# Optimization experiments

Hardware: AMD Instinct MI355X
Metric: run time of the kernel (lower is better)

Reference implementation:

```python
import jax, jax.numpy as jnp
import numpy as np

B, N, TOP_K = 4, 2048, 30
NUM_PE, NUM_RBF, EDGE_F = 16, 16, 128

def l2norm(x, eps=1e-12):
    return x / jnp.maximum(jnp.linalg.norm(x, axis=-1, keepdims=True), eps)

def gather_nodes(nodes, idx):
    # nodes [B,N,C], idx [B,N,K] -> [B,N,K,C]
    return jax.vmap(lambda n, i: n[i])(nodes, idx)

def setup_inputs() -> dict:
    key = jax.random.key(0)
    k1, k2 = jax.random.split(key)
    X = jax.random.normal(k1, (B, N, 3), dtype=jnp.float32) * 5.0
    mask = jnp.ones((B, N), dtype=jnp.float32)
    W = jax.random.normal(k2, (NUM_PE + NUM_RBF + 7, EDGE_F), dtype=jnp.float32) * 0.1
    b = jnp.zeros((EDGE_F,), dtype=jnp.float32)
    gamma = jnp.ones((EDGE_F,), dtype=jnp.float32)
    beta = jnp.zeros((EDGE_F,), dtype=jnp.float32)
    return {"X": X, "mask": mask, "W": W, "b": b, "gamma": gamma, "beta": beta}

def _quaternions(R):
    # R [B,N,K,3,3] -> Q [B,N,K,4]
    diag = jnp.diagonal(R, axis1=-2, axis2=-1)  # [B,N,K,3]
    Rxx, Ryy, Rzz = diag[..., 0], diag[..., 1], diag[..., 2]
    mags = 0.5 * jnp.sqrt(jnp.abs(1.0 + jnp.stack(
        [Rxx - Ryy - Rzz, -Rxx + Ryy - Rzz, -Rxx - Ryy + Rzz], -1)))
    signs = jnp.sign(jnp.stack([
        R[..., 2, 1] - R[..., 1, 2],
        R[..., 0, 2] - R[..., 2, 0],
        R[..., 1, 0] - R[..., 0, 1]], -1))
    xyz = signs * mags
    w = jnp.sqrt(jax.nn.relu(1.0 + jnp.sum(diag, -1, keepdims=True))) / 2.0
    Q = jnp.concatenate((xyz, w), -1)
    return l2norm(Q)

def _forward(X, mask, W, b, gamma, beta):
    eps = 1e-6
    # pairwise distances + top-k neighbors
    mask_2D = mask[:, None, :] * mask[:, :, None]
    dXp = X[:, None, :, :] - X[:, :, None, :]
    D = mask_2D * jnp.sqrt(jnp.sum(dXp ** 2, -1) + eps)
    D_max = jnp.max(D, -1, keepdims=True)
    D_adjust = D + (1.0 - mask_2D) * D_max
    neg_vals, E_idx = jax.lax.top_k(-D_adjust, TOP_K)
    D_neighbors = -neg_vals

    # RBF
    D_mu = jnp.linspace(0.0, 20.0, NUM_RBF)
    D_sigma = 20.0 / NUM_RBF
    RBF = jnp.exp(-(((D_neighbors[..., None] - D_mu) / D_sigma) ** 2))

    # orientations
    dX = X[:, 1:, :] - X[:, :-1, :]
    U = l2norm(dX)
    u_2, u_1 = U[:, :-2, :], U[:, 1:-1, :]
    n_2 = l2norm(jnp.cross(u_2, u_1))
    o_1 = l2norm(u_2 - u_1)
    O = jnp.stack((o_1, n_2, jnp.cross(o_1, n_2)), 2)  # [B,N-3,3,3]
    O9 = O.reshape(O.shape[0], O.shape[1], 9)
    O9 = jnp.pad(O9, ((0, 0), (1, 2), (0, 0)))  # [B,N,9]
    O_neighbors = gather_nodes(O9, E_idx).reshape(B, N, TOP_K, 3, 3)
    X_neighbors = gather_nodes(X, E_idx)  # [B,N,K,3]
    Om = O9.reshape(B, N, 3, 3)
    dXn = X_neighbors - X[:, :, None, :]
    dU = l2norm(jnp.einsum('bnij,bnkj->bnki', Om, dXn))
    R = jnp.einsum('bnji,bnkjl->bnkil', Om, O_neighbors)
    Q = _quaternions(R)
    O_features = jnp.concatenate((dU, Q), -1)  # [B,N,K,7]

    # positional encodings
    ii = jnp.arange(N, dtype=jnp.float32)[None, :, None]
    d = (E_idx.astype(jnp.float32) - ii)[..., None]
    freq = jnp.exp(jnp.arange(0, NUM_PE, 2, dtype=jnp.float32) * -(np.log(10000.0) / NUM_PE))
    angles = d * freq
    E_positional = jnp.concatenate((jnp.cos(angles), jnp.sin(angles)), -1)

    E = jnp.concatenate((E_positional, RBF, O_features), -1)  # [B,N,K,39]
    E = E @ W + b
    # Normalize (LayerNorm w/ unbiased std, as in struct2seq Normalize)
    mu = jnp.mean(E, -1, keepdims=True)
    sigma = jnp.sqrt(jnp.var(E, -1, keepdims=True, ddof=1) + eps)
    E = gamma * (E - mu) / (sigma + eps) + beta
    return E, E_idx

def reference(X, mask, W, b, gamma, beta):
    return _forward(X, mask, W, b, gamma, beta)
```

## Files before the change

kernel.cpp:

```cpp
#include <hip/hip_runtime.h>
#include <stdint.h>

#define B_ 4
#define N_ 2048
#define K_ 30
#define F_ 128
#define NF 39

typedef unsigned long long u64;
typedef float f32x4 __attribute__((ext_vector_type(4)));
typedef short s16x8 __attribute__((ext_vector_type(8)));

__device__ __forceinline__ u64 umin64(u64 a, u64 b) { return a < b ? a : b; }
__device__ __forceinline__ u64 umax64(u64 a, u64 b) { return a > b ? a : b; }

template <int CTRL>
__device__ __forceinline__ float dpp_add(float x) {
    int r = __builtin_amdgcn_update_dpp(0, __float_as_int(x), CTRL, 0xF, 0xF, true);
    return x + __int_as_float(r);
}
__device__ __forceinline__ float rowsum16(float x) {
    x = dpp_add<0xB1>(x);
    x = dpp_add<0x4E>(x);
    x = dpp_add<0x141>(x);
    x = dpp_add<0x140>(x);
    return x;
}

__device__ __forceinline__ unsigned int bf16rne(float f) {
    unsigned int u = __float_as_uint(f);
    return (u + 0x7FFFu + ((u >> 16) & 1u)) >> 16;
}
__device__ __forceinline__ unsigned int bfpack(float a, float b) {
    return bf16rne(a) | (bf16rne(b) << 16);
}

__global__ __launch_bounds__(256) void topk_kernel(const float* __restrict__ X,
                                                   float* __restrict__ O9,
                                                   int* __restrict__ Eidx,
                                                   float* __restrict__ Dn,
                                                   float* __restrict__ EidxF) {
    __shared__ float4 P[N_];
    __shared__ u64 surv[4][64];
    int t = threadIdx.x, lane = t & 63, wid = t >> 6;
    int node = blockIdx.x * 4 + wid;
    int i = node & (N_ - 1);
    const float* Xb = X + (size_t)(node - i) * 3;
    float* Pf = (float*)P;

    for (int idx = t; idx < 3 * N_; idx += 256) {
        float v = Xb[idx];
        int j = idx / 3, c = idx - 3 * j;
        Pf[4 * j + c] = v;
    }
    __syncthreads();

    if (t < 4) {
        int nn = blockIdx.x * 4 + t;
        int ii = nn & (N_ - 1);
        float o[9] = {0.f,0.f,0.f,0.f,0.f,0.f,0.f,0.f,0.f};
        if (ii >= 1 && ii <= N_ - 3) {
            float4 A = P[ii-1], Bv = P[ii], C = P[ii+1];
            float u2x = Bv.x-A.x, u2y = Bv.y-A.y, u2z = Bv.z-A.z;
            float n2_ = sqrtf(u2x*u2x+u2y*u2y+u2z*u2z);
            float inv = 1.0f / fmaxf(n2_, 1e-12f);
            u2x*=inv; u2y*=inv; u2z*=inv;
            float u1x = C.x-Bv.x, u1y = C.y-Bv.y, u1z = C.z-Bv.z;
            float n1_ = sqrtf(u1x*u1x+u1y*u1y+u1z*u1z);
            inv = 1.0f / fmaxf(n1_, 1e-12f);
            u1x*=inv; u1y*=inv; u1z*=inv;
            float nx = u2y*u1z - u2z*u1y;
            float ny = u2z*u1x - u2x*u1z;
            float nz = u2x*u1y - u2y*u1x;
            float nn2 = sqrtf(nx*nx+ny*ny+nz*nz);
            inv = 1.0f / fmaxf(nn2, 1e-12f);
            nx*=inv; ny*=inv; nz*=inv;
            float ox = u2x-u1x, oy = u2y-u1y, oz = u2z-u1z;
            float no = sqrtf(ox*ox+oy*oy+oz*oz);
            inv = 1.0f / fmaxf(no, 1e-12f);
            ox*=inv; oy*=inv; oz*=inv;
            o[0]=ox; o[1]=oy; o[2]=oz;
            o[3]=nx; o[4]=ny; o[5]=nz;
            o[6]=oy*nz - oz*ny; o[7]=oz*nx - ox*nz; o[8]=ox*ny - oy*nx;
        }
        float* dst = O9 + (size_t)nn * 9;
        #pragma unroll
        for (int q = 0; q < 9; ++q) dst[q] = o[q];
    }

    float4 ci = P[i];
    float xi = ci.x, yi = ci.y, zi = ci.z;

    unsigned int d[32];
    #pragma unroll
    for (int s = 0; s < 32; ++s) {
        float4 p = P[lane + (s << 6)];
        float dx = __fsub_rn(p.x, xi);
        float dy = __fsub_rn(p.y, yi);
        float dz = __fsub_rn(p.z, zi);
        float s1 = __fadd_rn(__fmul_rn(dx,dx), __fmul_rn(dy,dy));
        float s2 = __fadd_rn(s1, __fmul_rn(dz,dz));
        d[s] = __float_as_uint(__fadd_rn(s2, 1e-6f));
    }

    unsigned int lm = d[0];
    #pragma unroll
    for (int s = 1; s < 32; ++s) lm = min(lm, d[s]);

    unsigned int v32 = lm;
    #pragma unroll
    for (int k = 2; k <= 64; k <<= 1) {
        #pragma unroll
        for (int j = k >> 1; j >= 1; j >>= 1) {
            unsigned int o = (unsigned int)__shfl_xor((int)v32, j, 64);
            bool up = ((lane & k) == 0);
            bool lower = ((lane & j) == 0);
            v32 = (lower == up) ? min(v32, o) : max(v32, o);
        }
    }
    unsigned int Bcut = (unsigned int)__shfl((int)v32, K_ - 1, 64) + 64u;

    surv[wid][lane] = ~0ull;
    int base = 0;
    #pragma unroll
    for (int s = 0; s < 32; ++s) {
        bool p = (d[s] <= Bcut);
        u64 blt = __ballot(p);
        if (p) {
            int slot = base + (int)__popcll(blt & ((1ull << lane) - 1ull));
            if (slot < 64) {
                float D = __fsqrt_rn(__uint_as_float(d[s]));
                surv[wid][slot] = (((u64)__float_as_uint(D)) << 32)
                                | (unsigned int)(lane + (s << 6));
            }
        }
        base += (int)__popcll(blt);
    }
    int cnt = base;

    if (cnt <= 64) {
        u64 v = surv[wid][lane];
        #pragma unroll
        for (int k = 2; k <= 64; k <<= 1) {
            #pragma unroll
            for (int j = k >> 1; j >= 1; j >>= 1) {
                u64 o = (u64)__shfl_xor((long long)v, j, 64);
                bool up = ((lane & k) == 0);
                bool lower = ((lane & j) == 0);
                v = (lower == up) ? umin64(v, o) : umax64(v, o);
            }
        }
        if (lane < K_ && lane < cnt) {
            int j = (int)(v & 0xffffffffull);
            int o = node * K_ + lane;
            Eidx[o] = j;
            Dn[o] = __uint_as_float((unsigned int)(v >> 32));
            EidxF[o] = (float)j;
        }
    } else {
        #pragma unroll
        for (int s = 0; s < 32; ++s)
            d[s] = __float_as_uint(__fsqrt_rn(__uint_as_float(d[s])));
        for (int k = 0; k < K_; ++k) {
            u64 m = ~0ull;
            #pragma unroll
            for (int s = 0; s < 32; ++s) {
                u64 kk = (((u64)d[s]) << 32) | (unsigned int)(lane + (s << 6));
                m = umin64(m, kk);
            }
            #pragma unroll
            for (int off = 1; off < 64; off <<= 1)
                m = umin64(m, (u64)__shfl_xor((long long)m, off, 64));
            #pragma unroll
            for (int s = 0; s < 32; ++s) {
                u64 kk = (((u64)d[s]) << 32) | (unsigned int)(lane + (s << 6));
                if (kk == m) d[s] = 0xFFFFFFFFu;
            }
            if (lane == 0) {
                int o = node * K_ + k;
                int j = (int)(m & 0xffffffffull);
                Eidx[o] = j;
                Dn[o] = __uint_as_float((unsigned int)(m >> 32));
                EidxF[o] = (float)j;
            }
        }
    }
}

__global__ __launch_bounds__(256) void edge_fused(const float* __restrict__ X,
                                                  const float* __restrict__ O9,
                                                  const int* __restrict__ Eidx,
                                                  const float* __restrict__ Dn,
                                                  const float* __restrict__ W,
                                                  const float* __restrict__ bias,
                                                  const float* __restrict__ gamma,
                                                  const float* __restrict__ beta,
                                                  float* __restrict__ E) {
    __shared__ unsigned int ldsF[128 * 32];
    __shared__ unsigned int ldsW[128 * 32];
    int t = threadIdx.x, lane = t & 63, wid = t >> 6;
    int e0 = blockIdx.x * 128;

    if (t < 128) {
        int e = e0 + t;
        int b = e / (N_ * K_);
        int rem = e - b * (N_ * K_);
        int i = rem / K_;
        int node = b * N_ + i;
        int j = Eidx[e];
        float dnb = Dn[e];

        float f[40];
        float dd = (float)(j - i);
        const float freqs[8] = {1.0f, 0.31622776601683794f, 0.1f, 0.031622776601683794f,
                                0.01f, 0.0031622776601683794f, 0.001f, 0.00031622776601683794f};
        #pragma unroll
        for (int l = 0; l < 8; ++l) {
            float a = dd * freqs[l];
            float sv, cv;
            __sincosf(a, &sv, &cv);
            f[l] = cv;
            f[8 + l] = sv;
        }
        #pragma unroll
        for (int r = 0; r < 16; ++r) {
            float mu = (20.0f / 15.0f) * (float)r;
            float u = (dnb - mu) * 0.8f;
            f[16 + r] = __expf(-u * u);
        }
        const float* Omp = O9 + (size_t)node * 9;
        float Om[9];
        #pragma unroll
        for (int q = 0; q < 9; ++q) Om[q] = Omp[q];
        const float* Xi = X + (size_t)node * 3;
        const float* Xj = X + (size_t)(b * N_ + j) * 3;
        float dx = Xj[0] - Xi[0], dy = Xj[1] - Xi[1], dz = Xj[2] - Xi[2];
        float v0 = Om[0]*dx + Om[1]*dy + Om[2]*dz;
        float v1 = Om[3]*dx + Om[4]*dy + Om[5]*dz;
        float v2 = Om[6]*dx + Om[7]*dy + Om[8]*dz;
        float n = sqrtf(v0*v0 + v1*v1 + v2*v2);
        float inv = 1.0f / fmaxf(n, 1e-12f);
        f[32] = v0 * inv; f[33] = v1 * inv; f[34] = v2 * inv;
        const float* On = O9 + (size_t)(b * N_ + j) * 9;
        float R00 = Om[0]*On[0] + Om[3]*On[3] + Om[6]*On[6];
        float R01 = Om[0]*On[1] + Om[3]*On[4] + Om[6]*On[7];
        float R02 = Om[0]*On[2] + Om[3]*On[5] + Om[6]*On[8];
        float R10 = Om[1]*On[0] + Om[4]*On[3] + Om[7]*On[6];
        float R11 = Om[1]*On[1] + Om[4]*On[4] + Om[7]*On[7];
        float R12 = Om[1]*On[2] + Om[4]*On[5] + Om[7]*On[8];
        float R20 = Om[2]*On[0] + Om[5]*On[3] + Om[8]*On[6];
        float R21 = Om[2]*On[1] + Om[5]*On[4] + Om[8]*On[7];
        float R22 = Om[2]*On[2] + Om[5]*On[5] + Om[8]*On[8];
        float mg0 = 0.5f * sqrtf(fabsf(1.0f + R00 - R11 - R22));
        float mg1 = 0.5f * sqrtf(fabsf(1.0f - R00 + R11 - R22));
        float mg2 = 0.5f * sqrtf(fabsf(1.0f - R00 - R11 + R22));
        float t0 = R21 - R12, t1 = R02 - R20, t2 = R10 - R01;
        float s0 = (t0 > 0.f) ? 1.f : ((t0 < 0.f) ? -1.f : 0.f);
        float s1 = (t1 > 0.f) ? 1.f : ((t1 < 0.f) ? -1.f : 0.f);
        float s2 = (t2 > 0.f) ? 1.f : ((t2 < 0.f) ? -1.f : 0.f);
        float q0 = s0 * mg0, q1 = s1 * mg1, q2 = s2 * mg2;
        float w = sqrtf(fmaxf(1.0f + R00 + R11 + R22, 0.0f)) * 0.5f;
        float nq = sqrtf(q0*q0 + q1*q1 + q2*q2 + w*w);
        inv = 1.0f / fmaxf(nq, 1e-12f);
        f[35] = q0 * inv; f[36] = q1 * inv; f[37] = q2 * inv; f[38] = w * inv;
        f[39] = 0.0f;

        int row = t;
        #pragma unroll
        for (int c = 0; c < 8; ++c) {
            uint4 u;
            if (c < 5) {
                u.x = bfpack(f[8*c+0], f[8*c+1]);
                u.y = bfpack(f[8*c+2], f[8*c+3]);
                u.z = bfpack(f[8*c+4], f[8*c+5]);
                u.w = bfpack(f[8*c+6], f[8*c+7]);
            } else {
                u = make_uint4(0u, 0u, 0u, 0u);
            }
            int idx = row * 32 + ((4 * c) ^ ((row & 7) << 2));
            *(uint4*)&ldsF[idx] = u;
        }
    } else {
        int col = t - 128;
        #pragma unroll
        for (int c8 = 0; c8 < 8; ++c8) {
            uint4 u;
            unsigned int* up = (unsigned int*)&u;
            #pragma unroll
            for (int m = 0; m < 4; ++m) {
                int k0 = 8 * c8 + 2 * m, k1 = k0 + 1;
                float a  = (k0 < NF) ? W[k0 * F_ + col] : 0.f;
                float bv = (k1 < NF) ? W[k1 * F_ + col] : 0.f;
                up[m] = bfpack(a, bv);
            }
            int idx = col * 32 + ((4 * c8) ^ ((col & 7) << 2));
            *(uint4*)&ldsW[idx] = u;
        }
    }

    float gg[8], be8[8], bb[8];
    #pragma unroll
    for (int tt = 0; tt < 8; ++tt) {
        int c = 16 * tt + (lane & 15);
        gg[tt] = gamma[c]; be8[tt] = beta[c]; bb[tt] = bias[c];
    }

    __syncthreads();

    s16x8 wf[8][2];
    #pragma unroll
    for (int tt = 0; tt < 8; ++tt) {
        int col = 16 * tt + (lane & 15);
        #pragma unroll
        for (int s = 0; s < 2; ++s) {
            int idx = col * 32 + ((((lane >> 4) * 4) + s * 16) ^ ((col & 7) << 2));
            wf[tt][s] = *(s16x8*)&ldsW[idx];
        }
    }

    #pragma unroll
    for (int wt = 0; wt < 2; ++wt) {
        int ebase = wid * 32 + wt * 16;
        int arow = ebase + (lane & 15);
        s16x8 af[2];
        #pragma unroll
        for (int s = 0; s < 2; ++s) {
            int idx = arow * 32 + ((((lane >> 4) * 4) + s * 16) ^ ((arow & 7) << 2));
            af[s] = *(s16x8*)&ldsF[idx];
        }
        f32x4 acc[8];
        #pragma unroll
        for (int tt = 0; tt < 8; ++tt) {
            acc[tt] = (f32x4){0.f, 0.f, 0.f, 0.f};
            acc[tt] = __builtin_amdgcn_mfma_f32_16x16x32_bf16(af[0], wf[tt][0], acc[tt], 0, 0, 0);
            acc[tt] = __builtin_amdgcn_mfma_f32_16x16x32_bf16(af[1], wf[tt][1], acc[tt], 0, 0, 0);
        }
        float sum[4] = {0,0,0,0}, sq[4] = {0,0,0,0};
        #pragma unroll
        for (int tt = 0; tt < 8; ++tt) {
            #pragma unroll
            for (int q = 0; q < 4; ++q) {
                float v = acc[tt][q] + bb[tt];
                acc[tt][q] = v;
                sum[q] += v;
                sq[q] = fmaf(v, v, sq[q]);
            }
        }
        float muv[4], invv[4];
        #pragma unroll
        for (int q = 0; q < 4; ++q) {
            float S  = rowsum16(sum[q]);
            float Qs = rowsum16(sq[q]);
            float mu = S * (1.0f / 128.0f);
            float var = (Qs - S * mu) * (1.0f / 127.0f);
            muv[q] = mu;
            invv[q] = 1.0f / (sqrtf(var + 1e-6f) + 1e-6f);
        }
        size_t base = (size_t)(e0 + ebase) * F_;
        #pragma unroll
        for (int tt = 0; tt < 8; ++tt) {
            int c = 16 * tt + (lane & 15);
            #pragma unroll
            for (int q = 0; q < 4; ++q) {
                int er = (lane >> 4) * 4 + q;
                E[base + (size_t)er * F_ + c] =
                    gg[tt] * (acc[tt][q] - muv[q]) * invv[q] + be8[tt];
            }
        }
    }
}

extern "C" void kernel_launch(void* const* d_in, const int* in_sizes, int n_in,
                              void* d_out, int out_size, void* d_ws, size_t ws_size,
                              hipStream_t stream) {
    const float* X     = (const float*)d_in[0];
    const float* W     = (const float*)d_in[2];
    const float* bias  = (const float*)d_in[3];
    const float* gamma = (const float*)d_in[4];
    const float* beta  = (const float*)d_in[5];

    float* E      = (float*)d_out;
    float* EidxF  = (float*)d_out + (size_t)B_ * N_ * K_ * F_;

    float* O9   = (float*)d_ws;
    int*   Eidx = (int*)(O9 + (size_t)B_ * N_ * 9);
    float* Dn   = (float*)(Eidx + (size_t)B_ * N_ * K_);

    int nodes = B_ * N_;
    int edges = nodes * K_;

    hipLaunchKernelGGL(topk_kernel, dim3(nodes / 4), dim3(256), 0, stream,
                       X, O9, Eidx, Dn, EidxF);
    hipLaunchKernelGGL(edge_fused, dim3(edges / 128), dim3(256), 0, stream,
                       X, O9, Eidx, Dn, W, bias, gamma, beta, E);
}
```

Before: 51.01 us.

## Fuse top-k selection and edge feature MLP into a single kernel

Merges the neighbor-selection kernel and the edge feature/projection/LayerNorm kernel into one launch, where each block handles four nodes and their thirty edges. Neighbor indices and distances stay in shared memory, and the orientation frames are recomputed from the shared coordinate buffer instead of going through a global workspace. This removes a kernel launch and global round trips for intermediates. In exchange, shared memory is aliased between coordinates and GEMM tiles, and the MFMA tiles are padded from 30 to 32 rows per node.

```diff
diff --git a/kernel.cpp b/kernel.cpp
--- a/kernel.cpp
+++ b/kernel.cpp
@@ -35,13 +35,50 @@
     return bf16rne(a) | (bf16rne(b) << 16);
 }
 
-__global__ __launch_bounds__(256) void topk_kernel(const float* __restrict__ X,
-                                                   float* __restrict__ O9,
-                                                   int* __restrict__ Eidx,
-                                                   float* __restrict__ Dn,
-                                                   float* __restrict__ EidxF) {
-    __shared__ float4 P[N_];
+__device__ __forceinline__ void frame_from(const float4* Pp, int ii, float o[9]) {
+    #pragma unroll
+    for (int q = 0; q < 9; ++q) o[q] = 0.f;
+    if (ii >= 1 && ii <= N_ - 3) {
+        float4 A = Pp[ii-1], Bv = Pp[ii], C = Pp[ii+1];
+        float u2x = Bv.x-A.x, u2y = Bv.y-A.y, u2z = Bv.z-A.z;
+        float n2_ = sqrtf(u2x*u2x+u2y*u2y+u2z*u2z);
+        float inv = 1.0f / fmaxf(n2_, 1e-12f);
+        u2x*=inv; u2y*=inv; u2z*=inv;
+        float u1x = C.x-Bv.x, u1y = C.y-Bv.y, u1z = C.z-Bv.z;
+        float n1_ = sqrtf(u1x*u1x+u1y*u1y+u1z*u1z);
+        inv = 1.0f / fmaxf(n1_, 1e-12f);
+        u1x*=inv; u1y*=inv; u1z*=inv;
+        float nx = u2y*u1z - u2z*u1y;
+        float ny = u2z*u1x - u2x*u1z;
+        float nz = u2x*u1y - u2y*u1x;
+        float nn2 = sqrtf(nx*nx+ny*ny+nz*nz);
+        inv = 1.0f / fmaxf(nn2, 1e-12f);
+        nx*=inv; ny*=inv; nz*=inv;
+        float ox = u2x-u1x, oy = u2y-u1y, oz = u2z-u1z;
+        float no = sqrtf(ox*ox+oy*oy+oz*oz);
+        inv = 1.0f / fmaxf(no, 1e-12f);
+        ox*=inv; oy*=inv; oz*=inv;
+        o[0]=ox; o[1]=oy; o[2]=oz;
+        o[3]=nx; o[4]=ny; o[5]=nz;
+        o[6]=oy*nz - oz*ny; o[7]=oz*nx - ox*nz; o[8]=ox*ny - oy*nx;
+    }
+}
+
+__global__ __launch_bounds__(256) void fused_kernel(const float* __restrict__ X,
+                                                    const float* __restrict__ W,
+                                                    const float* __restrict__ bias,
+                                                    const float* __restrict__ gamma,
+                                                    const float* __restrict__ beta,
+                                                    float* __restrict__ E,
+                                                    float* __restrict__ EidxF) {
+    __shared__ __align__(16) unsigned char shraw[32768];
+    float4* P = (float4*)shraw;
+    unsigned int* ldsF = (unsigned int*)shraw;
+    unsigned int* ldsW = (unsigned int*)(shraw + 16384);
     __shared__ u64 surv[4][64];
+    __shared__ int   idxL[4][32];
+    __shared__ float DL[4][32];
+
     int t = threadIdx.x, lane = t & 63, wid = t >> 6;
     int node = blockIdx.x * 4 + wid;
     int i = node & (N_ - 1);
@@ -54,39 +91,6 @@
         Pf[4 * j + c] = v;
     }
     __syncthreads();
-
-    if (t < 4) {
-        int nn = blockIdx.x * 4 + t;
-        int ii = nn & (N_ - 1);
-        float o[9] = {0.f,0.f,0.f,0.f,0.f,0.f,0.f,0.f,0.f};
-        if (ii >= 1 && ii <= N_ - 3) {
-            float4 A = P[ii-1], Bv = P[ii], C = P[ii+1];
-            float u2x = Bv.x-A.x, u2y = Bv.y-A.y, u2z = Bv.z-A.z;
-            float n2_ = sqrtf(u2x*u2x+u2y*u2y+u2z*u2z);
-            float inv = 1.0f / fmaxf(n2_, 1e-12f);
-            u2x*=inv; u2y*=inv; u2z*=inv;
-            float u1x = C.x-Bv.x, u1y = C.y-Bv.y, u1z = C.z-Bv.z;
-            float n1_ = sqrtf(u1x*u1x+u1y*u1y+u1z*u1z);
-            inv = 1.0f / fmaxf(n1_, 1e-12f);
-            u1x*=inv; u1y*=inv; u1z*=inv;
-            float nx = u2y*u1z - u2z*u1y;
-            float ny = u2z*u1x - u2x*u1z;
-            float nz = u2x*u1y - u2y*u1x;
-            float nn2 = sqrtf(nx*nx+ny*ny+nz*nz);
-            inv = 1.0f / fmaxf(nn2, 1e-12f);
-            nx*=inv; ny*=inv; nz*=inv;
-            float ox = u2x-u1x, oy = u2y-u1y, oz = u2z-u1z;
-            float no = sqrtf(ox*ox+oy*oy+oz*oz);
-            inv = 1.0f / fmaxf(no, 1e-12f);
-            ox*=inv; oy*=inv; oz*=inv;
-            o[0]=ox; o[1]=oy; o[2]=oz;
-            o[3]=nx; o[4]=ny; o[5]=nz;
-            o[6]=oy*nz - oz*ny; o[7]=oz*nx - ox*nz; o[8]=ox*ny - oy*nx;
-        }
-        float* dst = O9 + (size_t)nn * 9;
-        #pragma unroll
-        for (int q = 0; q < 9; ++q) dst[q] = o[q];
-    }
 
     float4 ci = P[i];
     float xi = ci.x, yi = ci.y, zi = ci.z;
@@ -150,12 +154,11 @@
                 v = (lower == up) ? umin64(v, o) : umax64(v, o);
             }
         }
-        if (lane < K_ && lane < cnt) {
+        if (lane < K_) {
             int j = (int)(v & 0xffffffffull);
-            int o = node * K_ + lane;
-            Eidx[o] = j;
-            Dn[o] = __uint_as_float((unsigned int)(v >> 32));
-            EidxF[o] = (float)j;
+            idxL[wid][lane] = j;
+            DL[wid][lane] = __uint_as_float((unsigned int)(v >> 32));
+            EidxF[node * K_ + lane] = (float)j;
         }
     } else {
         #pragma unroll
@@ -177,41 +180,32 @@
                 if (kk == m) d[s] = 0xFFFFFFFFu;
             }
             if (lane == 0) {
-                int o = node * K_ + k;
                 int j = (int)(m & 0xffffffffull);
-                Eidx[o] = j;
-                Dn[o] = __uint_as_float((unsigned int)(m >> 32));
-                EidxF[o] = (float)j;
-            }
-        }
-    }
-}
-
-__global__ __launch_bounds__(256) void edge_fused(const float* __restrict__ X,
-                                                  const float* __restrict__ O9,
-                                                  const int* __restrict__ Eidx,
-                                                  const float* __restrict__ Dn,
-                                                  const float* __restrict__ W,
-                                                  const float* __restrict__ bias,
-                                                  const float* __restrict__ gamma,
-                                                  const float* __restrict__ beta,
-                                                  float* __restrict__ E) {
-    __shared__ unsigned int ldsF[128 * 32];
-    __shared__ unsigned int ldsW[128 * 32];
-    int t = threadIdx.x, lane = t & 63, wid = t >> 6;
-    int e0 = blockIdx.x * 128;
-
-    if (t < 128) {
-        int e = e0 + t;
-        int b = e / (N_ * K_);
-        int rem = e - b * (N_ * K_);
-        int i = rem / K_;
-        int node = b * N_ + i;
-        int j = Eidx[e];
-        float dnb = Dn[e];
+                idxL[wid][k] = j;
+                DL[wid][k] = __uint_as_float((unsigned int)(m >> 32));
+                EidxF[node * K_ + k] = (float)j;
+            }
+        }
+    }
+    __syncthreads();
+
+    uint4 fpack[5];
+    uint4 wreg[8];
+    float gg[8], be8[8], bb[8];
+    #pragma unroll
+    for (int tt = 0; tt < 8; ++tt) {
+        int c = 16 * tt + (lane & 15);
+        gg[tt] = gamma[c]; be8[tt] = beta[c]; bb[tt] = bias[c];
+    }
+
+    if (t < 120) {
+        int nl = t / 30, k = t - nl * 30;
+        int il = (blockIdx.x * 4 + nl) & (N_ - 1);
+        int j = idxL[nl][k];
+        float dnb = DL[nl][k];
 
         float f[40];
-        float dd = (float)(j - i);
+        float dd = (float)(j - il);
         const float freqs[8] = {1.0f, 0.31622776601683794f, 0.1f, 0.031622776601683794f,
                                 0.01f, 0.0031622776601683794f, 0.001f, 0.00031622776601683794f};
         #pragma unroll
@@ -228,20 +222,17 @@
             float u = (dnb - mu) * 0.8f;
             f[16 + r] = __expf(-u * u);
         }
-        const float* Omp = O9 + (size_t)node * 9;
-        float Om[9];
-        #pragma unroll
-        for (int q = 0; q < 9; ++q) Om[q] = Omp[q];
-        const float* Xi = X + (size_t)node * 3;
-        const float* Xj = X + (size_t)(b * N_ + j) * 3;
-        float dx = Xj[0] - Xi[0], dy = Xj[1] - Xi[1], dz = Xj[2] - Xi[2];
+        float Om[9], On[9];
+        frame_from(P, il, Om);
+        frame_from(P, j, On);
+        float4 Pi = P[il], Pj = P[j];
+        float dx = Pj.x - Pi.x, dy = Pj.y - Pi.y, dz = Pj.z - Pi.z;
         float v0 = Om[0]*dx + Om[1]*dy + Om[2]*dz;
         float v1 = Om[3]*dx + Om[4]*dy + Om[5]*dz;
         float v2 = Om[6]*dx + Om[7]*dy + Om[8]*dz;
         float n = sqrtf(v0*v0 + v1*v1 + v2*v2);
         float inv = 1.0f / fmaxf(n, 1e-12f);
         f[32] = v0 * inv; f[33] = v1 * inv; f[34] = v2 * inv;
-        const float* On = O9 + (size_t)(b * N_ + j) * 9;
         float R00 = Om[0]*On[0] + Om[3]*On[3] + Om[6]*On[6];
         float R01 = Om[0]*On[1] + Om[3]*On[4] + Om[6]*On[7];
         float R02 = Om[0]*On[2] + Om[3]*On[5] + Om[6]*On[8];
@@ -265,27 +256,18 @@
         f[35] = q0 * inv; f[36] = q1 * inv; f[37] = q2 * inv; f[38] = w * inv;
         f[39] = 0.0f;
 
-        int row = t;
-        #pragma unroll
-        for (int c = 0; c < 8; ++c) {
-            uint4 u;
-            if (c < 5) {
-                u.x = bfpack(f[8*c+0], f[8*c+1]);
-                u.y = bfpack(f[8*c+2], f[8*c+3]);
-                u.z = bfpack(f[8*c+4], f[8*c+5]);
-                u.w = bfpack(f[8*c+6], f[8*c+7]);
-            } else {
-                u = make_uint4(0u, 0u, 0u, 0u);
-            }
-            int idx = row * 32 + ((4 * c) ^ ((row & 7) << 2));
-            *(uint4*)&ldsF[idx] = u;
-        }
-    } else {
+        #pragma unroll
+        for (int c = 0; c < 5; ++c) {
+            fpack[c].x = bfpack(f[8*c+0], f[8*c+1]);
+            fpack[c].y = bfpack(f[8*c+2], f[8*c+3]);
+            fpack[c].z = bfpack(f[8*c+4], f[8*c+5]);
+            fpack[c].w = bfpack(f[8*c+6], f[8*c+7]);
+        }
+    } else if (t >= 128) {
         int col = t - 128;
         #pragma unroll
         for (int c8 = 0; c8 < 8; ++c8) {
-            uint4 u;
-            unsigned int* up = (unsigned int*)&u;
+            unsigned int* up = (unsigned int*)&wreg[c8];
             #pragma unroll
             for (int m = 0; m < 4; ++m) {
                 int k0 = 8 * c8 + 2 * m, k1 = k0 + 1;
@@ -293,18 +275,27 @@
                 float bv = (k1 < NF) ? W[k1 * F_ + col] : 0.f;
                 up[m] = bfpack(a, bv);
             }
+        }
+    }
+    __syncthreads();
+
+    if (t < 120) {
+        int nl = t / 30, k = t - nl * 30;
+        int row = nl * 32 + k;
+        #pragma unroll
+        for (int c = 0; c < 8; ++c) {
+            uint4 u = (c < 5) ? fpack[c] : make_uint4(0u, 0u, 0u, 0u);
+            int idx = row * 32 + ((4 * c) ^ ((row & 7) << 2));
+            *(uint4*)&ldsF[idx] = u;
+        }
+    } else if (t >= 128) {
+        int col = t - 128;
+        #pragma unroll
+        for (int c8 = 0; c8 < 8; ++c8) {
             int idx = col * 32 + ((4 * c8) ^ ((col & 7) << 2));
-            *(uint4*)&ldsW[idx] = u;
-        }
-    }
-
-    float gg[8], be8[8], bb[8];
-    #pragma unroll
-    for (int tt = 0; tt < 8; ++tt) {
-        int c = 16 * tt + (lane & 15);
-        gg[tt] = gamma[c]; be8[tt] = beta[c]; bb[tt] = bias[c];
-    }
-
+            *(uint4*)&ldsW[idx] = wreg[c8];
+        }
+    }
     __syncthreads();
 
     s16x8 wf[8][2];
@@ -318,10 +309,10 @@
         }
     }
 
+    size_t rowbase_g = (size_t)blockIdx.x * 120 + wid * 30;
     #pragma unroll
     for (int wt = 0; wt < 2; ++wt) {
-        int ebase = wid * 32 + wt * 16;
-        int arow = ebase + (lane & 15);
+        int arow = wid * 32 + wt * 16 + (lane & 15);
         s16x8 af[2];
         #pragma unroll
         for (int s = 0; s < 2; ++s) {
@@ -356,15 +347,16 @@
             muv[q] = mu;
             invv[q] = 1.0f / (sqrtf(var + 1e-6f) + 1e-6f);
         }
-        size_t base = (size_t)(e0 + ebase) * F_;
         #pragma unroll
         for (int tt = 0; tt < 8; ++tt) {
             int c = 16 * tt + (lane & 15);
             #pragma unroll
             for (int q = 0; q < 4; ++q) {
-                int er = (lane >> 4) * 4 + q;
-                E[base + (size_t)er * F_ + c] =
-                    gg[tt] * (acc[tt][q] - muv[q]) * invv[q] + be8[tt];
+                int local_k = wt * 16 + (lane >> 4) * 4 + q;
+                if (local_k < K_) {
+                    E[(rowbase_g + local_k) * F_ + c] =
+                        gg[tt] * (acc[tt][q] - muv[q]) * invv[q] + be8[tt];
+                }
             }
         }
     }
@@ -382,15 +374,8 @@
     float* E      = (float*)d_out;
     float* EidxF  = (float*)d_out + (size_t)B_ * N_ * K_ * F_;
 
-    float* O9   = (float*)d_ws;
-    int*   Eidx = (int*)(O9 + (size_t)B_ * N_ * 9);
-    float* Dn   = (float*)(Eidx + (size_t)B_ * N_ * K_);
-
     int nodes = B_ * N_;
-    int edges = nodes * K_;
-
-    hipLaunchKernelGGL(topk_kernel, dim3(nodes / 4), dim3(256), 0, stream,
-                       X, O9, Eidx, Dn, EidxF);
-    hipLaunchKernelGGL(edge_fused, dim3(edges / 128), dim3(256), 0, stream,
-                       X, O9, Eidx, Dn, W, bias, gamma, beta, E);
-}
+
+    hipLaunchKernelGGL(fused_kernel, dim3(nodes / 4), dim3(256), 0, stream,
+                       X, W, bias, gamma, beta, E, EidxF);
+}
```

Result: slower. 61.24 us (+20.0%).
